# Performance work log

Measured on AMD Instinct MI355X. Metric: run time of the kernel, lower is better.

Reference implementation:

```python
import jax, jax.numpy as jnp
import numpy as np

B, L, D = 4, 2048, 1024
H, DK, DV = 16, 64, 64


def setup_inputs() -> dict:
    key = jax.random.key(0)
    ks = jax.random.split(key, 11)
    s = 1.0 / np.sqrt(D)
    so = 1.0 / np.sqrt(H * DV)
    return {
        "query": jax.random.normal(ks[0], (B, L, D), jnp.float32),
        "key": jax.random.normal(ks[1], (B, L, D), jnp.float32),
        "value": jax.random.normal(ks[2], (B, L, D), jnp.float32),
        "W_q": jax.random.uniform(ks[3], (D, H * DK), jnp.float32, -s, s),
        "b_q": jax.random.uniform(ks[4], (H * DK,), jnp.float32, -s, s),
        "W_k": jax.random.uniform(ks[5], (D, H * DK), jnp.float32, -s, s),
        "b_k": jax.random.uniform(ks[6], (H * DK,), jnp.float32, -s, s),
        "W_v": jax.random.uniform(ks[7], (D, H * DV), jnp.float32, -s, s),
        "b_v": jax.random.uniform(ks[8], (H * DV,), jnp.float32, -s, s),
        "W_o": jax.random.uniform(ks[9], (H * DV, D), jnp.float32, -so, so),
        "b_o": jax.random.uniform(ks[10], (D,), jnp.float32, -so, so),
    }


def reference(query, key, value, W_q, b_q, W_k, b_k, W_v, b_v, W_o, b_o):
    # QKV projections, then split heads: [B, L, H*d] -> [B, H, L, d]
    q = (query @ W_q + b_q).reshape(B, L, H, DK).transpose(0, 2, 1, 3)
    k = (key @ W_k + b_k).reshape(B, L, H, DK).transpose(0, 2, 1, 3)
    v = (value @ W_v + b_v).reshape(B, L, H, DV).transpose(0, 2, 1, 3)
    # scaled dot-product attention: softmax(q k^T / sqrt(dk)) v
    scores = jnp.einsum("bhqd,bhkd->bhqk", q, k) / jnp.sqrt(jnp.float32(DK))
    attn = jax.nn.softmax(scores, axis=-1)
    ctx = jnp.einsum("bhqk,bhkd->bhqd", attn, v)
    # combine heads: [B, H, L, dv] -> [B, L, H*dv], output projection
    out = ctx.transpose(0, 2, 1, 3).reshape(B, L, H * DV) @ W_o + b_o
    return out
```

## Files before the change

### kernel.cpp

```cpp
#include <hip/hip_runtime.h>

#define BATCH 4
#define LSEQ 2048
#define DMODEL 1024
#define NHEAD 16
#define DHEAD 64
#define MTOT (BATCH * LSEQ)

typedef _Float16 f16;
typedef _Float16 f16x8 __attribute__((ext_vector_type(8)));
typedef _Float16 f16x4 __attribute__((ext_vector_type(4)));
typedef float f32x4 __attribute__((ext_vector_type(4)));

#define SCORE_SCALE 0.180336878f

typedef const __attribute__((address_space(1))) void gvoid;
typedef __attribute__((address_space(3))) void lvoid;
#define GLDS16(g, l) __builtin_amdgcn_global_load_lds((gvoid*)(g), (lvoid*)(l), 16, 0, 0)

__global__ __launch_bounds__(256)
void cvt3_f32_f16(const float* __restrict__ in0, const float* __restrict__ in1,
                  const float* __restrict__ in2, f16* __restrict__ out, int n8)
{
    const int y = blockIdx.y;
    const float* in = (y == 0) ? in0 : (y == 1) ? in1 : in2;
    f16* o = out + (size_t)y * (size_t)n8 * 8;
    int i = blockIdx.x * 256 + threadIdx.x;
    if (i >= n8) return;
    float4 a = ((const float4*)in)[2 * i];
    float4 b = ((const float4*)in)[2 * i + 1];
    f16x8 v;
    v[0] = (f16)a.x; v[1] = (f16)a.y; v[2] = (f16)a.z; v[3] = (f16)a.w;
    v[4] = (f16)b.x; v[5] = (f16)b.y; v[6] = (f16)b.z; v[7] = (f16)b.w;
    ((f16x8*)o)[i] = v;
}

__global__ __launch_bounds__(256)
void wconv4(const float* __restrict__ W0, const float* __restrict__ W1,
            const float* __restrict__ W2, const float* __restrict__ W3,
            f16* __restrict__ WtBase)
{
    __shared__ float T[64][68];
    const int z = blockIdx.z;
    const float* W = (z == 0) ? W0 : (z == 1) ? W1 : (z == 2) ? W2 : W3;
    f16* Wt = WtBase + (size_t)z * DMODEL * DMODEL;
    const int t = threadIdx.x;
    const int k0 = blockIdx.y * 64, n0 = blockIdx.x * 64;
    const int tr = t >> 4, tc = (t & 15) * 4;
#pragma unroll
    for (int p = 0; p < 64; p += 16) {
        float4 v = *(const float4*)&W[(size_t)(k0 + tr + p) * DMODEL + n0 + tc];
        *(float4*)&T[tr + p][tc] = v;
    }
    __syncthreads();
    const int n = t >> 2, kc = (t & 3) * 16;
    f16x8 o0, o1;
#pragma unroll
    for (int j = 0; j < 8; ++j) o0[j] = (f16)T[kc + j][n];
#pragma unroll
    for (int j = 0; j < 8; ++j) o1[j] = (f16)T[kc + 8 + j][n];
    *(f16x8*)&Wt[(size_t)(n0 + n) * DMODEL + k0 + kc] = o0;
    *(f16x8*)&Wt[(size_t)(n0 + n) * DMODEL + k0 + kc + 8] = o1;
}

__global__ __launch_bounds__(256)
void gemm_f16(const f16* __restrict__ A, const f16* __restrict__ Bt,
              const float* __restrict__ b0, const float* __restrict__ b1,
              const float* __restrict__ b2, void* __restrict__ Cout, int fused)
{
    __shared__ f16 As2[2][128][32];
    __shared__ f16 Bs2[2][128][32];

    const int t = threadIdx.x;
    const int lane = t & 63, w = t >> 6;
    const int quad = lane >> 4, m16 = lane & 15;
    const int m0 = blockIdx.x * 128;
    const int n0 = blockIdx.y * 128;
    const int wm = (w & 1) * 64, wn = (w >> 1) * 64;

    const int which = fused ? (n0 >> 10) : 0;

    f32x4 acc[4][4] = {};

    const f16* Ag = A + (size_t)which * MTOT * DMODEL
                      + (size_t)(m0 + (t >> 2)) * DMODEL + (t & 3) * 8;
    const f16* Bg = Bt + (size_t)(n0 + (t >> 2)) * DMODEL + (t & 3) * 8;
    f16* Al = &As2[0][0][0] + t * 8;
    f16* Bl = &Bs2[0][0][0] + t * 8;

    for (int k0 = 0; k0 < DMODEL; k0 += 64) {
        __syncthreads();
#pragma unroll
        for (int h = 0; h < 2; ++h) {
            GLDS16(Ag + k0 + h * 32, Al + h * 4096);
            GLDS16(Ag + k0 + h * 32 + (size_t)64 * DMODEL, Al + h * 4096 + 2048);
            GLDS16(Bg + k0 + h * 32, Bl + h * 4096);
            GLDS16(Bg + k0 + h * 32 + (size_t)64 * DMODEL, Bl + h * 4096 + 2048);
        }
        __syncthreads();
#pragma unroll
        for (int h = 0; h < 2; ++h) {
            f16x8 af[4], bf[4];
#pragma unroll
            for (int mi = 0; mi < 4; ++mi)
                af[mi] = *(const f16x8*)&As2[h][wm + mi * 16 + m16][quad * 8];
#pragma unroll
            for (int ni = 0; ni < 4; ++ni)
                bf[ni] = *(const f16x8*)&Bs2[h][wn + ni * 16 + m16][quad * 8];
#pragma unroll
            for (int mi = 0; mi < 4; ++mi)
#pragma unroll
                for (int ni = 0; ni < 4; ++ni)
                    acc[mi][ni] = __builtin_amdgcn_mfma_f32_16x16x32_f16(
                        af[mi], bf[ni], acc[mi][ni], 0, 0, 0);
        }
    }

    if (fused) {
        const float* bp = (which == 0) ? b0 : (which == 1) ? b1 : b2;
        const float scale = (which == 0) ? SCORE_SCALE : 1.0f;
        f16* o = (f16*)Cout + (size_t)which * MTOT * DMODEL;
#pragma unroll
        for (int ni = 0; ni < 4; ++ni) {
            const int nn = (n0 + wn + ni * 16 + m16) & 1023;
            const float bv = bp[nn];
            const int h = nn >> 6, d = nn & 63;
#pragma unroll
            for (int mi = 0; mi < 4; ++mi) {
                const int mrow = m0 + wm + mi * 16 + quad * 4;
                const int b = mrow >> 11, l0 = mrow & (LSEQ - 1);
                if (which < 2) {
#pragma unroll
                    for (int j = 0; j < 4; ++j) {
                        const float v = (acc[mi][ni][j] + bv) * scale;
                        o[(((size_t)(b * NHEAD + h) * LSEQ + l0 + j) << 6) + d] = (f16)v;
                    }
                } else {
                    f16x4 pk;
#pragma unroll
                    for (int j = 0; j < 4; ++j) pk[j] = (f16)(acc[mi][ni][j] + bv);
                    *(f16x4*)&o[(((size_t)(b * NHEAD + h) << 6) + d) * LSEQ + l0] = pk;
                }
            }
        }
    } else {
#pragma unroll
        for (int ni = 0; ni < 4; ++ni) {
            const int n = n0 + wn + ni * 16 + m16;
            const float bv = b0[n];
#pragma unroll
            for (int mi = 0; mi < 4; ++mi)
#pragma unroll
                for (int j = 0; j < 4; ++j) {
                    const int m = m0 + wm + mi * 16 + quad * 4 + j;
                    ((float*)Cout)[(size_t)m * DMODEL + n] = acc[mi][ni][j] + bv;
                }
        }
    }
}

__global__ __launch_bounds__(256, 2)
void attn_mfma(const f16* __restrict__ Qh, const f16* __restrict__ Kh,
               const f16* __restrict__ Vt, f16* __restrict__ ctx)
{
    __shared__ f16 Ks[2][64][32];
    __shared__ f16 Vs[2][64][32];
    __shared__ f16 Ps[256][72];

    const int t = threadIdx.x;
    const int lane = t & 63, w = t >> 6;
    const int quad = lane >> 4, m16 = lane & 15;

    const int bid = blockIdx.x;
    const int x = bid & 7, rest = bid >> 3;
    const int qt = rest & 7;
    const int g = x + 8 * (rest >> 3);
    const int q0 = qt * 256, wq = w * 64;

    const f16* Qg = Qh + (size_t)g * LSEQ * DHEAD;
    const f16* Kg = Kh + (size_t)g * LSEQ * DHEAD;
    const f16* Vg = Vt + (size_t)g * LSEQ * DHEAD;

    f16x8 qa[4][2];
#pragma unroll
    for (int qi = 0; qi < 4; ++qi)
#pragma unroll
        for (int ks = 0; ks < 2; ++ks)
            qa[qi][ks] = *(const f16x8*)&Qg[(size_t)(q0 + wq + qi * 16 + m16) * DHEAD
                                            + ks * 32 + quad * 8];

    f32x4 ctxa[4][4] = {};
    float lsum[4] = {0.f, 0.f, 0.f, 0.f};

    const f16* ksrc = Kg + (size_t)(t >> 2) * DHEAD + (t & 3) * 8;
    const f16* vsrc = Vg + (size_t)(t >> 2) * LSEQ + (t & 3) * 8;
    f16* kdst = &Ks[0][0][0] + t * 8;
    f16* vdst = &Vs[0][0][0] + t * 8;

    for (int kt = 0; kt < LSEQ; kt += 64) {
        __syncthreads();
        GLDS16(ksrc + (size_t)kt * DHEAD, kdst);
        GLDS16(ksrc + (size_t)kt * DHEAD + 32, kdst + 2048);
        GLDS16(vsrc + kt, vdst);
        GLDS16(vsrc + kt + 32, vdst + 2048);
        __syncthreads();

        f16x8 kb[4][2];
#pragma unroll
        for (int ki = 0; ki < 4; ++ki)
#pragma unroll
            for (int ks = 0; ks < 2; ++ks)
                kb[ki][ks] = *(const f16x8*)&Ks[ks][ki * 16 + m16][quad * 8];

        f32x4 s[4][4];
#pragma unroll
        for (int ki = 0; ki < 4; ++ki)
#pragma unroll
            for (int qi = 0; qi < 4; ++qi) {
                f32x4 z = {0.f, 0.f, 0.f, 0.f};
                z = __builtin_amdgcn_mfma_f32_16x16x32_f16(kb[ki][0], qa[qi][0], z, 0, 0, 0);
                s[ki][qi] = __builtin_amdgcn_mfma_f32_16x16x32_f16(kb[ki][1], qa[qi][1], z, 0, 0, 0);
            }

#pragma unroll
        for (int ki = 0; ki < 4; ++ki)
#pragma unroll
            for (int qi = 0; qi < 4; ++qi) {
                f16x4 pk;
#pragma unroll
                for (int j = 0; j < 4; ++j) {
                    const float p = __builtin_amdgcn_exp2f(s[ki][qi][j]);
                    lsum[qi] += p;
                    pk[j] = (f16)p;
                }
                *(f16x4*)&Ps[wq + qi * 16 + m16][ki * 16 + quad * 4] = pk;
            }

        f16x8 pa[4][2], vb[4][2];
#pragma unroll
        for (int qi = 0; qi < 4; ++qi)
#pragma unroll
            for (int ks = 0; ks < 2; ++ks)
                pa[qi][ks] = *(const f16x8*)&Ps[wq + qi * 16 + m16][ks * 32 + quad * 8];
#pragma unroll
        for (int di = 0; di < 4; ++di)
#pragma unroll
            for (int ks = 0; ks < 2; ++ks)
                vb[di][ks] = *(const f16x8*)&Vs[ks][di * 16 + m16][quad * 8];
#pragma unroll
        for (int qi = 0; qi < 4; ++qi)
#pragma unroll
            for (int di = 0; di < 4; ++di) {
                ctxa[qi][di] = __builtin_amdgcn_mfma_f32_16x16x32_f16(pa[qi][0], vb[di][0], ctxa[qi][di], 0, 0, 0);
                ctxa[qi][di] = __builtin_amdgcn_mfma_f32_16x16x32_f16(pa[qi][1], vb[di][1], ctxa[qi][di], 0, 0, 0);
            }
    }

    float linv[4];
#pragma unroll
    for (int qi = 0; qi < 4; ++qi) {
        float l = lsum[qi];
        l += __shfl_xor(l, 16);
        l += __shfl_xor(l, 32);
        linv[qi] = 1.0f / l;
    }

    const int batch = g >> 4, h = g & 15;
#pragma unroll
    for (int qi = 0; qi < 4; ++qi)
#pragma unroll
        for (int j = 0; j < 4; ++j) {
            const float inv = __shfl(linv[qi], quad * 4 + j);
            const int l = q0 + wq + qi * 16 + quad * 4 + j;
#pragma unroll
            for (int di = 0; di < 4; ++di) {
                const int col = h * 64 + di * 16 + m16;
                ctx[((size_t)batch * LSEQ + l) * DMODEL + col] = (f16)(ctxa[qi][di][j] * inv);
            }
        }
}

extern "C" void kernel_launch(void* const* d_in, const int* in_sizes, int n_in,
                              void* d_out, int out_size, void* d_ws, size_t ws_size,
                              hipStream_t stream)
{
    const float* query = (const float*)d_in[0];
    const float* key   = (const float*)d_in[1];
    const float* value = (const float*)d_in[2];
    const float* W_q   = (const float*)d_in[3];
    const float* b_q   = (const float*)d_in[4];
    const float* W_k   = (const float*)d_in[5];
    const float* b_k   = (const float*)d_in[6];
    const float* W_v   = (const float*)d_in[7];
    const float* b_v   = (const float*)d_in[8];
    const float* W_o   = (const float*)d_in[9];
    const float* b_o   = (const float*)d_in[10];
    float* out = (float*)d_out;

    const size_t MAT = (size_t)MTOT * DMODEL;
    f16* base = (f16*)d_ws;
    f16* Aq   = base;
    f16* Qhp  = base + 3 * MAT;
    f16* ctxh = base + 6 * MAT;
    f16* Wtq  = base + 7 * MAT;
    f16* Wto  = Wtq + (size_t)3 * DMODEL * DMODEL;

    const int n8 = (int)(MAT / 8);
    cvt3_f32_f16<<<dim3(n8 / 256, 3), 256, 0, stream>>>(query, key, value, Aq, n8);
    wconv4<<<dim3(DMODEL / 64, DMODEL / 64, 4), 256, 0, stream>>>(W_q, W_k, W_v, W_o, Wtq);

    gemm_f16<<<dim3(MTOT / 128, 3 * DMODEL / 128), 256, 0, stream>>>(
        Aq, Wtq, b_q, b_k, b_v, Qhp, 1);

    attn_mfma<<<BATCH * NHEAD * (LSEQ / 256), 256, 0, stream>>>(
        Qhp, Qhp + MAT, Qhp + 2 * MAT, ctxh);

    gemm_f16<<<dim3(MTOT / 128, DMODEL / 128), 256, 0, stream>>>(
        ctxh, Wto, b_o, nullptr, nullptr, out, 0);
}
```

Measured before the change: 332.6 us.

## Fuse fp32-to-fp16 input conversion into QKV GEMM and double-buffer GEMM/attention loads

Removes the standalone fp32→fp16 conversion kernel. The QKV GEMM now loads fp32 activations into registers, converts them and writes them to LDS itself. Both GEMMs switch to a 32-wide K step with LDS double buffering and prefetch of the next tile, and the attention kernel double-buffers its K/V tiles so the next tile's loads overlap compute. This saves a full read and write of the three activation tensors. In exchange the fused GEMM reads fp32 A through registers (twice the bytes per tile, repeated for every N-tile block), and it adds launch_bounds(256,4), which may cap registers.

```diff
diff --git a/kernel.cpp b/kernel.cpp
--- a/kernel.cpp
+++ b/kernel.cpp
@@ -18,21 +18,12 @@
 typedef __attribute__((address_space(3))) void lvoid;
 #define GLDS16(g, l) __builtin_amdgcn_global_load_lds((gvoid*)(g), (lvoid*)(l), 16, 0, 0)
 
-__global__ __launch_bounds__(256)
-void cvt3_f32_f16(const float* __restrict__ in0, const float* __restrict__ in1,
-                  const float* __restrict__ in2, f16* __restrict__ out, int n8)
-{
-    const int y = blockIdx.y;
-    const float* in = (y == 0) ? in0 : (y == 1) ? in1 : in2;
-    f16* o = out + (size_t)y * (size_t)n8 * 8;
-    int i = blockIdx.x * 256 + threadIdx.x;
-    if (i >= n8) return;
-    float4 a = ((const float4*)in)[2 * i];
-    float4 b = ((const float4*)in)[2 * i + 1];
-    f16x8 v;
-    v[0] = (f16)a.x; v[1] = (f16)a.y; v[2] = (f16)a.z; v[3] = (f16)a.w;
-    v[4] = (f16)b.x; v[5] = (f16)b.y; v[6] = (f16)b.z; v[7] = (f16)b.w;
-    ((f16x8*)o)[i] = v;
+__device__ __forceinline__ f16x8 pack8(float4 a, float4 b)
+{
+    f16x8 r;
+    r[0] = (f16)a.x; r[1] = (f16)a.y; r[2] = (f16)a.z; r[3] = (f16)a.w;
+    r[4] = (f16)b.x; r[5] = (f16)b.y; r[6] = (f16)b.z; r[7] = (f16)b.w;
+    return r;
 }
 
 __global__ __launch_bounds__(256)
@@ -63,8 +54,10 @@
     *(f16x8*)&Wt[(size_t)(n0 + n) * DMODEL + k0 + kc + 8] = o1;
 }
 
-__global__ __launch_bounds__(256)
-void gemm_f16(const f16* __restrict__ A, const f16* __restrict__ Bt,
+__global__ __launch_bounds__(256, 4)
+void gemm_f16(const float* __restrict__ Aq32, const float* __restrict__ Ak32,
+              const float* __restrict__ Av32, const f16* __restrict__ A16,
+              const f16* __restrict__ Bt,
               const float* __restrict__ b0, const float* __restrict__ b1,
               const float* __restrict__ b2, void* __restrict__ Cout, int fused)
 {
@@ -82,37 +75,63 @@
 
     f32x4 acc[4][4] = {};
 
-    const f16* Ag = A + (size_t)which * MTOT * DMODEL
-                      + (size_t)(m0 + (t >> 2)) * DMODEL + (t & 3) * 8;
-    const f16* Bg = Bt + (size_t)(n0 + (t >> 2)) * DMODEL + (t & 3) * 8;
-    f16* Al = &As2[0][0][0] + t * 8;
-    f16* Bl = &Bs2[0][0][0] + t * 8;
-
-    for (int k0 = 0; k0 < DMODEL; k0 += 64) {
+    const float* A32 = (which == 0) ? Aq32 : (which == 1) ? Ak32 : Av32;
+    const float* Ag32 = fused ? (A32 + (size_t)(m0 + (t >> 2)) * DMODEL + (t & 3) * 8) : nullptr;
+    const f16*   Ag16 = fused ? nullptr : (A16 + (size_t)(m0 + (t >> 2)) * DMODEL + (t & 3) * 8);
+    const f16*   Bg   = Bt + (size_t)(n0 + (t >> 2)) * DMODEL + (t & 3) * 8;
+    f16* AlB = &As2[0][0][0] + t * 8;
+    f16* BlB = &Bs2[0][0][0] + t * 8;
+
+    if (fused) {
+        float4 p0 = *(const float4*)(Ag32);
+        float4 p1 = *(const float4*)(Ag32 + 4);
+        float4 p2 = *(const float4*)(Ag32 + (size_t)64 * DMODEL);
+        float4 p3 = *(const float4*)(Ag32 + (size_t)64 * DMODEL + 4);
+        *(f16x8*)(AlB) = pack8(p0, p1);
+        *(f16x8*)(AlB + 2048) = pack8(p2, p3);
+    } else {
+        GLDS16(Ag16, AlB);
+        GLDS16(Ag16 + (size_t)64 * DMODEL, AlB + 2048);
+    }
+    GLDS16(Bg, BlB);
+    GLDS16(Bg + (size_t)64 * DMODEL, BlB + 2048);
+
+    float4 ar0, ar1, ar2, ar3;
+
+    for (int k0 = 0; k0 < DMODEL; k0 += 32) {
+        const int buf = (k0 >> 5) & 1, nb = buf ^ 1;
+        const bool more = (k0 + 32 < DMODEL);
         __syncthreads();
-#pragma unroll
-        for (int h = 0; h < 2; ++h) {
-            GLDS16(Ag + k0 + h * 32, Al + h * 4096);
-            GLDS16(Ag + k0 + h * 32 + (size_t)64 * DMODEL, Al + h * 4096 + 2048);
-            GLDS16(Bg + k0 + h * 32, Bl + h * 4096);
-            GLDS16(Bg + k0 + h * 32 + (size_t)64 * DMODEL, Bl + h * 4096 + 2048);
-        }
-        __syncthreads();
-#pragma unroll
-        for (int h = 0; h < 2; ++h) {
-            f16x8 af[4], bf[4];
-#pragma unroll
-            for (int mi = 0; mi < 4; ++mi)
-                af[mi] = *(const f16x8*)&As2[h][wm + mi * 16 + m16][quad * 8];
+        if (more) {
+            const int kn = k0 + 32;
+            if (fused) {
+                ar0 = *(const float4*)(Ag32 + kn);
+                ar1 = *(const float4*)(Ag32 + kn + 4);
+                ar2 = *(const float4*)(Ag32 + kn + (size_t)64 * DMODEL);
+                ar3 = *(const float4*)(Ag32 + kn + (size_t)64 * DMODEL + 4);
+            } else {
+                GLDS16(Ag16 + kn, AlB + nb * 4096);
+                GLDS16(Ag16 + kn + (size_t)64 * DMODEL, AlB + nb * 4096 + 2048);
+            }
+            GLDS16(Bg + kn, BlB + nb * 4096);
+            GLDS16(Bg + kn + (size_t)64 * DMODEL, BlB + nb * 4096 + 2048);
+        }
+        f16x8 af[4], bf[4];
+#pragma unroll
+        for (int mi = 0; mi < 4; ++mi)
+            af[mi] = *(const f16x8*)&As2[buf][wm + mi * 16 + m16][quad * 8];
+#pragma unroll
+        for (int ni = 0; ni < 4; ++ni)
+            bf[ni] = *(const f16x8*)&Bs2[buf][wn + ni * 16 + m16][quad * 8];
+#pragma unroll
+        for (int mi = 0; mi < 4; ++mi)
 #pragma unroll
             for (int ni = 0; ni < 4; ++ni)
-                bf[ni] = *(const f16x8*)&Bs2[h][wn + ni * 16 + m16][quad * 8];
-#pragma unroll
-            for (int mi = 0; mi < 4; ++mi)
-#pragma unroll
-                for (int ni = 0; ni < 4; ++ni)
-                    acc[mi][ni] = __builtin_amdgcn_mfma_f32_16x16x32_f16(
-                        af[mi], bf[ni], acc[mi][ni], 0, 0, 0);
+                acc[mi][ni] = __builtin_amdgcn_mfma_f32_16x16x32_f16(
+                    af[mi], bf[ni], acc[mi][ni], 0, 0, 0);
+        if (more && fused) {
+            *(f16x8*)(AlB + nb * 4096) = pack8(ar0, ar1);
+            *(f16x8*)(AlB + nb * 4096 + 2048) = pack8(ar2, ar3);
         }
     }
 
@@ -163,8 +182,8 @@
 void attn_mfma(const f16* __restrict__ Qh, const f16* __restrict__ Kh,
                const f16* __restrict__ Vt, f16* __restrict__ ctx)
 {
-    __shared__ f16 Ks[2][64][32];
-    __shared__ f16 Vs[2][64][32];
+    __shared__ f16 Ks[2][2][64][32];
+    __shared__ f16 Vs[2][2][64][32];
     __shared__ f16 Ps[256][72];
 
     const int t = threadIdx.x;
@@ -194,23 +213,31 @@
 
     const f16* ksrc = Kg + (size_t)(t >> 2) * DHEAD + (t & 3) * 8;
     const f16* vsrc = Vg + (size_t)(t >> 2) * LSEQ + (t & 3) * 8;
-    f16* kdst = &Ks[0][0][0] + t * 8;
-    f16* vdst = &Vs[0][0][0] + t * 8;
+    f16* kdstB = &Ks[0][0][0][0] + t * 8;
+    f16* vdstB = &Vs[0][0][0][0] + t * 8;
+
+    GLDS16(ksrc, kdstB);
+    GLDS16(ksrc + 32, kdstB + 2048);
+    GLDS16(vsrc, vdstB);
+    GLDS16(vsrc + 32, vdstB + 2048);
 
     for (int kt = 0; kt < LSEQ; kt += 64) {
+        const int buf = (kt >> 6) & 1, nb = buf ^ 1;
         __syncthreads();
-        GLDS16(ksrc + (size_t)kt * DHEAD, kdst);
-        GLDS16(ksrc + (size_t)kt * DHEAD + 32, kdst + 2048);
-        GLDS16(vsrc + kt, vdst);
-        GLDS16(vsrc + kt + 32, vdst + 2048);
-        __syncthreads();
+        if (kt + 64 < LSEQ) {
+            const size_t ko = (size_t)(kt + 64);
+            GLDS16(ksrc + ko * DHEAD, kdstB + nb * 4096);
+            GLDS16(ksrc + ko * DHEAD + 32, kdstB + nb * 4096 + 2048);
+            GLDS16(vsrc + ko, vdstB + nb * 4096);
+            GLDS16(vsrc + ko + 32, vdstB + nb * 4096 + 2048);
+        }
 
         f16x8 kb[4][2];
 #pragma unroll
         for (int ki = 0; ki < 4; ++ki)
 #pragma unroll
             for (int ks = 0; ks < 2; ++ks)
-                kb[ki][ks] = *(const f16x8*)&Ks[ks][ki * 16 + m16][quad * 8];
+                kb[ki][ks] = *(const f16x8*)&Ks[buf][ks][ki * 16 + m16][quad * 8];
 
         f32x4 s[4][4];
 #pragma unroll
@@ -246,7 +273,7 @@
         for (int di = 0; di < 4; ++di)
 #pragma unroll
             for (int ks = 0; ks < 2; ++ks)
-                vb[di][ks] = *(const f16x8*)&Vs[ks][di * 16 + m16][quad * 8];
+                vb[di][ks] = *(const f16x8*)&Vs[buf][ks][di * 16 + m16][quad * 8];
 #pragma unroll
         for (int qi = 0; qi < 4; ++qi)
 #pragma unroll
@@ -299,22 +326,19 @@
 
     const size_t MAT = (size_t)MTOT * DMODEL;
     f16* base = (f16*)d_ws;
-    f16* Aq   = base;
-    f16* Qhp  = base + 3 * MAT;
-    f16* ctxh = base + 6 * MAT;
-    f16* Wtq  = base + 7 * MAT;
+    f16* Qhp  = base;
+    f16* ctxh = base + 3 * MAT;
+    f16* Wtq  = base + 4 * MAT;
     f16* Wto  = Wtq + (size_t)3 * DMODEL * DMODEL;
 
-    const int n8 = (int)(MAT / 8);
-    cvt3_f32_f16<<<dim3(n8 / 256, 3), 256, 0, stream>>>(query, key, value, Aq, n8);
     wconv4<<<dim3(DMODEL / 64, DMODEL / 64, 4), 256, 0, stream>>>(W_q, W_k, W_v, W_o, Wtq);
 
     gemm_f16<<<dim3(MTOT / 128, 3 * DMODEL / 128), 256, 0, stream>>>(
-        Aq, Wtq, b_q, b_k, b_v, Qhp, 1);
+        query, key, value, nullptr, Wtq, b_q, b_k, b_v, Qhp, 1);
 
     attn_mfma<<<BATCH * NHEAD * (LSEQ / 256), 256, 0, stream>>>(
         Qhp, Qhp + MAT, Qhp + 2 * MAT, ctxh);
 
     gemm_f16<<<dim3(MTOT / 128, DMODEL / 128), 256, 0, stream>>>(
-        ctxh, Wto, b_o, nullptr, nullptr, out, 0);
-}
+        nullptr, nullptr, nullptr, ctxh, Wto, b_o, nullptr, nullptr, out, 0);
+}
```

Result: slower. 355.8 us (+7.0%).
